# Optimization experiments

Hardware: AMD Instinct MI355X
Metric: run time of the kernel (lower is better)

Reference implementation:

```python
import jax, jax.numpy as jnp
import numpy as np

D_MODEL = 256; N_HEADS = 8; D_FFN = 1024; N_LEVELS = 4; N_POINTS = 4
HEAD_DIM = D_MODEL // N_HEADS
SHAPES = ((100, 100), (50, 50), (25, 25), (13, 13))  # static (H, W) per level
LEN_V = sum(h * w for h, w in SHAPES)  # 13294
BS = 8; NQ = 900


def layer_norm(x, g, b, eps=1e-5):
    m = x.mean(-1, keepdims=True)
    v = ((x - m) ** 2).mean(-1, keepdims=True)
    return (x - m) * jax.lax.rsqrt(v + eps) * g + b


def bilinear_sample(val, loc, H, W):
    # val: [bs, nH, H*W, hd]; loc: [bs, nq, nH, P, 2] normalized to [0,1].
    # Matches torch grid_sample(bilinear, zeros padding, align_corners=False)
    # with grid = 2*loc - 1, i.e. pixel coords x = loc_x*W - 0.5.
    bs, nq, nH, P, _ = loc.shape
    x = loc[..., 0] * W - 0.5
    y = loc[..., 1] * H - 0.5
    x0 = jnp.floor(x); y0 = jnp.floor(y)
    fx = x - x0; fy = y - y0  # grads flow to loc through fx/fy
    x0 = x0.astype(jnp.int32); y0 = y0.astype(jnp.int32)
    out = jnp.zeros((bs, nq, nH, P, HEAD_DIM), val.dtype)
    for dy, wy in ((0, 1.0 - fy), (1, fy)):
        for dx, wx in ((0, 1.0 - fx), (1, fx)):
            xi = x0 + dx; yi = y0 + dy
            valid = (xi >= 0) & (xi < W) & (yi >= 0) & (yi < H)
            idx = jnp.clip(yi, 0, H - 1) * W + jnp.clip(xi, 0, W - 1)  # [bs,nq,nH,P]
            idx = idx.transpose(0, 2, 1, 3).reshape(bs, nH, nq * P)
            g = jnp.take_along_axis(val, idx[..., None], axis=2)  # [bs,nH,nq*P,hd]
            g = g.reshape(bs, nH, nq, P, HEAD_DIM).transpose(0, 2, 1, 3, 4)
            w = (wx * wy * valid).astype(val.dtype)[..., None]
            out = out + g * w
    return out  # [bs, nq, nH, P, hd]


def setup_inputs() -> dict:
    key = jax.random.key(0)
    ks = jax.random.split(key, 16)
    d = D_MODEL
    w = lambda k, shape: (jax.random.normal(k, shape) * 0.02).astype(jnp.float32)
    z = lambda n: jnp.zeros((n,), jnp.float32)
    o = lambda n: jnp.ones((n,), jnp.float32)
    return {
        "embed": jax.random.normal(ks[0], (BS, NQ, d), jnp.float32),
        "refer_bbox": jax.random.uniform(ks[1], (BS, NQ, 4), jnp.float32),  # cxcywh in [0,1]
        "feats": jax.random.normal(ks[2], (BS, LEN_V, d), jnp.float32),
        "query_pos": jax.random.normal(ks[3], (BS, NQ, d), jnp.float32),
        "Wq": w(ks[4], (d, d)), "bq": z(d), "Wk": w(ks[5], (d, d)), "bk": z(d),
        "Wv": w(ks[6], (d, d)), "bv": z(d), "Wo": w(ks[7], (d, d)), "bo": z(d),
        "g1": o(d), "b1": z(d),
        "Wval": w(ks[8], (d, d)), "bval": z(d),
        "Woff": w(ks[9], (d, N_HEADS * N_LEVELS * N_POINTS * 2)), "boff": z(N_HEADS * N_LEVELS * N_POINTS * 2),
        "Waw": w(ks[10], (d, N_HEADS * N_LEVELS * N_POINTS)), "baw": z(N_HEADS * N_LEVELS * N_POINTS),
        "Wop": w(ks[11], (d, d)), "bop": z(d),
        "g2": o(d), "b2": z(d),
        "W1": w(ks[12], (d, D_FFN)), "bf1": z(D_FFN),
        "W2": w(ks[13], (D_FFN, d)), "bf2": z(d),
        "g3": o(d), "b3": z(d),
    }


def reference(embed, refer_bbox, feats, query_pos, Wq, bq, Wk, bk, Wv, bv, Wo, bo,
              g1, b1, Wval, bval, Woff, boff, Waw, baw, Wop, bop, g2, b2,
              W1, bf1, W2, bf2, g3, b3):
    bs, nq, d = embed.shape
    # ---- self attention (q = k = embed + query_pos, v = embed) ----
    qk_in = embed + query_pos
    q = (qk_in @ Wq + bq).reshape(bs, nq, N_HEADS, HEAD_DIM)
    k = (qk_in @ Wk + bk).reshape(bs, nq, N_HEADS, HEAD_DIM)
    v = (embed @ Wv + bv).reshape(bs, nq, N_HEADS, HEAD_DIM)
    scores = jnp.einsum('bqhd,bkhd->bhqk', q, k) * (HEAD_DIM ** -0.5)
    attn = jax.nn.softmax(scores, -1)
    sa = jnp.einsum('bhqk,bkhd->bqhd', attn, v).reshape(bs, nq, d) @ Wo + bo
    embed = layer_norm(embed + sa, g1, b1)
    # ---- MSDeformAttn cross attention ----
    query = embed + query_pos
    rb = refer_bbox[:, :, None, :]  # [bs, nq, 1, 4] (refer_bbox.unsqueeze(2))
    value = (feats @ Wval + bval).reshape(bs, LEN_V, N_HEADS, HEAD_DIM)
    off = (query @ Woff + boff).reshape(bs, nq, N_HEADS, N_LEVELS, N_POINTS, 2)
    aw = jax.nn.softmax((query @ Waw + baw).reshape(bs, nq, N_HEADS, N_LEVELS * N_POINTS), -1)
    aw = aw.reshape(bs, nq, N_HEADS, N_LEVELS, N_POINTS)
    # num_points == 4 branch: loc = cxcy + off/P * wh * 0.5
    loc = rb[:, :, None, :, None, :2] + off / N_POINTS * rb[:, :, None, :, None, 2:] * 0.5
    out = jnp.zeros((bs, nq, N_HEADS, HEAD_DIM), embed.dtype)
    start = 0
    for l, (H, W) in enumerate(SHAPES):
        val_l = value[:, start:start + H * W].transpose(0, 2, 1, 3)  # [bs,nH,HW,hd]
        s = bilinear_sample(val_l, loc[:, :, :, l], H, W)  # [bs,nq,nH,P,hd]
        out = out + (s * aw[:, :, :, l, :, None]).sum(3)
        start += H * W
    ca = out.reshape(bs, nq, d) @ Wop + bop
    embed = layer_norm(embed + ca, g2, b2)
    # ---- FFN ----
    ff = jax.nn.relu(embed @ W1 + bf1) @ W2 + bf2
    return layer_norm(embed + ff, g3, b3)
```

## Files before the change

kernel.cpp:

```cpp
#include <hip/hip_runtime.h>
#include <hip/hip_bf16.h>
#include <cstddef>

#define BS 8
#define NQ 900
#define DM 256
#define LEN_V 13294

using bf16x8 = __attribute__((ext_vector_type(8))) __bf16;
using f32x4  = __attribute__((ext_vector_type(4))) float;

__device__ __forceinline__ unsigned short f2bf(float f) {
    union { float f; unsigned int u; } v; v.f = f;
    unsigned int r = v.u + 0x7FFFu + ((v.u >> 16) & 1u);
    return (unsigned short)(r >> 16);
}
__device__ __forceinline__ float bf2f(unsigned short u) {
    union { unsigned int u; float f; } v; v.u = ((unsigned int)u) << 16;
    return v.f;
}

#define SW(r) (((r) + ((r) >> 2)) & 3)

#define FLAG_RELU 1
#define FLAG_OBF  2
#define FLAG_SWAP 4
#define FLAG_QKV  8

struct WDesc { const float* src; unsigned short* dst; int K; int N; float scale; };
struct WPrepArgs { WDesc w[10]; };

__global__ __launch_bounds__(256) void wprep_kernel(WPrepArgs args)
{
    WDesc d = args.w[blockIdx.z];
    int k0 = blockIdx.x * 32;
    int n0 = blockIdx.y * 32;
    if (k0 >= d.K || n0 >= d.N) return;
    __shared__ unsigned short t[32][33];
    int tx = threadIdx.x & 31, ty = threadIdx.x >> 5;
    #pragma unroll
    for (int i = 0; i < 4; ++i) {
        int kk = ty + i * 8;
        t[kk][tx] = f2bf(d.src[(size_t)(k0 + kk) * d.N + n0 + tx] * d.scale);
    }
    __syncthreads();
    #pragma unroll
    for (int i = 0; i < 4; ++i) {
        int nn = ty + i * 8;
        d.dst[(size_t)(n0 + nn) * d.K + k0 + tx] = t[tx][nn];
    }
}

__global__ __launch_bounds__(256) void bias_concat_kernel(
    const float* __restrict__ bq, const float* __restrict__ bk,
    const float* __restrict__ bv, const float* __restrict__ boff,
    const float* __restrict__ baw, float* __restrict__ bqkv,
    float* __restrict__ boffaw)
{
    const float sc = 0.17677669529663687f;
    int t = blockIdx.x * 256 + threadIdx.x;
    if (t < 256)       bqkv[t] = bq[t] * sc;
    else if (t < 512)  bqkv[t] = bk[t - 256];
    else if (t < 768)  bqkv[t] = bv[t - 512];
    if (t < 256)       boffaw[t] = boff[t];
    else if (t < 384)  boffaw[t] = baw[t - 256];
}

#define GLOADA(B, k0) do {                                                    \
    if constexpr (ABF) {                                                      \
        const unsigned short* ap_ = Abf + (size_t)agr * K + (k0) + ah;        \
        qa##B##0 = aok ? *(const uint4*)ap_ : z4;                             \
        qa##B##1 = aok ? *(const uint4*)(ap_ + 8) : z4;                       \
    } else {                                                                  \
        if (aok) {                                                            \
            const float* ap_ = Afp + (size_t)agr * K + (k0) + ah;             \
            pa##B##0 = *(const f32x4*)(ap_);                                  \
            pa##B##1 = *(const f32x4*)(ap_ + 4);                              \
            pa##B##2 = *(const f32x4*)(ap_ + 8);                              \
            pa##B##3 = *(const f32x4*)(ap_ + 12);                             \
            if (A2) {                                                         \
                const float* a2_ = A2 + (size_t)agr * K + (k0) + ah;          \
                pa##B##0 += *(const f32x4*)(a2_);                             \
                pa##B##1 += *(const f32x4*)(a2_ + 4);                         \
                pa##B##2 += *(const f32x4*)(a2_ + 8);                         \
                pa##B##3 += *(const f32x4*)(a2_ + 12);                        \
            }                                                                 \
        } else { pa##B##0 = zf4; pa##B##1 = zf4; pa##B##2 = zf4; pa##B##3 = zf4; } \
    }                                                                         \
    { const unsigned short* bp_ = BT + (size_t)bgr * K + (k0) + ah;           \
      pb##B##0 = *(const uint4*)bp_; pb##B##1 = *(const uint4*)(bp_ + 8); }   \
} while (0)

#define GSTAGE(B) do {                                                        \
    if constexpr (ABF) {                                                      \
        As4[ar * 4 + ((acb + 0) ^ SW(ar))] = qa##B##0;                        \
        As4[ar * 4 + ((acb + 1) ^ SW(ar))] = qa##B##1;                        \
    } else {                                                                  \
        union { unsigned short us_[8]; uint4 q_; } u0_, u1_;                  \
        u0_.us_[0] = f2bf(pa##B##0[0]); u0_.us_[1] = f2bf(pa##B##0[1]);       \
        u0_.us_[2] = f2bf(pa##B##0[2]); u0_.us_[3] = f2bf(pa##B##0[3]);       \
        u0_.us_[4] = f2bf(pa##B##1[0]); u0_.us_[5] = f2bf(pa##B##1[1]);       \
        u0_.us_[6] = f2bf(pa##B##1[2]); u0_.us_[7] = f2bf(pa##B##1[3]);       \
        u1_.us_[0] = f2bf(pa##B##2[0]); u1_.us_[1] = f2bf(pa##B##2[1]);       \
        u1_.us_[2] = f2bf(pa##B##2[2]); u1_.us_[3] = f2bf(pa##B##2[3]);       \
        u1_.us_[4] = f2bf(pa##B##3[0]); u1_.us_[5] = f2bf(pa##B##3[1]);       \
        u1_.us_[6] = f2bf(pa##B##3[2]); u1_.us_[7] = f2bf(pa##B##3[3]);       \
        As4[ar * 4 + ((acb + 0) ^ SW(ar))] = u0_.q_;                          \
        As4[ar * 4 + ((acb + 1) ^ SW(ar))] = u1_.q_;                          \
    }                                                                         \
    Bs4[ar * 4 + ((acb + 0) ^ SW(ar))] = pb##B##0;                            \
    Bs4[ar * 4 + ((acb + 1) ^ SW(ar))] = pb##B##1;                            \
} while (0)

#define GMFMA() do {                                                          \
    bf16x8 af[4], bfr[4];                                                     \
    _Pragma("unroll")                                                         \
    for (int mi = 0; mi < 4; ++mi) {                                          \
        int r = wm * 64 + mi * 16 + lr;                                       \
        af[mi] = Asb[r * 4 + (lc ^ SW(r))];                                   \
    }                                                                         \
    _Pragma("unroll")                                                         \
    for (int ni = 0; ni < 4; ++ni) {                                          \
        int r = wn * 64 + ni * 16 + lr;                                       \
        bfr[ni] = Bsb[r * 4 + (lc ^ SW(r))];                                  \
    }                                                                         \
    _Pragma("unroll")                                                         \
    for (int mi = 0; mi < 4; ++mi)                                            \
        _Pragma("unroll")                                                     \
        for (int ni = 0; ni < 4; ++ni)                                        \
            acc[mi][ni] = __builtin_amdgcn_mfma_f32_16x16x32_bf16(            \
                af[mi], bfr[ni], acc[mi][ni], 0, 0, 0);                       \
} while (0)

template<int ABF>
__global__ __launch_bounds__(256) void gemm_big(
    const void* __restrict__ Ain, const float* __restrict__ A2,
    const unsigned short* __restrict__ BT, const float* __restrict__ bias,
    void* __restrict__ Cout, int M, int N, int K, int flags)
{
    __shared__ uint4 SMEM[1088];
    uint4* As4 = SMEM;
    uint4* Bs4 = SMEM + 512;

    const int tid = threadIdx.x;
    const int lane = tid & 63;
    const int wave = tid >> 6;
    const int wm = wave >> 1;
    const int wn = wave & 1;
    const int row0 = (flags & FLAG_SWAP ? blockIdx.y : blockIdx.x) * 128;
    const int col0 = (flags & FLAG_SWAP ? blockIdx.x : blockIdx.y) * 128;
    if ((flags & FLAG_QKV) && col0 >= 512) A2 = nullptr;

    const float* Afp = (const float*)Ain;
    const unsigned short* Abf = (const unsigned short*)Ain;

    f32x4 acc[4][4];
    #pragma unroll
    for (int i = 0; i < 4; ++i)
        #pragma unroll
        for (int j = 0; j < 4; ++j)
            acc[i][j] = {0.f, 0.f, 0.f, 0.f};

    const int ar  = tid >> 1;
    const int ah  = (tid & 1) * 16;
    const int acb = (tid & 1) * 2;
    const int agr = row0 + ar;
    const bool aok = agr < M;
    const int bgr = col0 + ar;
    const int lr = lane & 15;
    const int lc = lane >> 4;

    const bf16x8* Asb = (const bf16x8*)As4;
    const bf16x8* Bsb = (const bf16x8*)Bs4;
    const uint4 z4 = {0u, 0u, 0u, 0u};
    const f32x4 zf4 = {0.f, 0.f, 0.f, 0.f};

    f32x4 pa00, pa01, pa02, pa03, pa10, pa11, pa12, pa13;
    uint4 qa00, qa01, qa10, qa11;
    uint4 pb00, pb01, pb10, pb11;

    const int nsteps = K >> 5;
    GLOADA(0, 0);
    for (int s = 0; s < nsteps; s += 2) {
        __syncthreads();
        GSTAGE(0);
        GLOADA(1, (s + 1 < nsteps ? (s + 1) * 32 : 0));
        __syncthreads();
        GMFMA();
        __syncthreads();
        GSTAGE(1);
        GLOADA(0, (s + 2 < nsteps ? (s + 2) * 32 : 0));
        __syncthreads();
        GMFMA();
    }

    const int relu = flags & FLAG_RELU;
    if (!(flags & FLAG_OBF)) {
        float* C = (float*)Cout;
        #pragma unroll
        for (int ni = 0; ni < 4; ++ni) {
            int col = col0 + wn * 64 + ni * 16 + lr;
            if (col >= N) continue;
            float bval = bias[col];
            #pragma unroll
            for (int mi = 0; mi < 4; ++mi) {
                #pragma unroll
                for (int rg = 0; rg < 4; ++rg) {
                    int row = row0 + wm * 64 + mi * 16 + lc * 4 + rg;
                    if (row < M) {
                        float o = acc[mi][ni][rg] + bval;
                        if (relu) o = fmaxf(o, 0.f);
                        C[(size_t)row * N + col] = o;
                    }
                }
            }
        }
    } else {
        unsigned short* RP = (unsigned short*)SMEM;
        unsigned short* C = (unsigned short*)Cout;
        float bval[4];
        #pragma unroll
        for (int ni = 0; ni < 4; ++ni) {
            int col = col0 + wn * 64 + ni * 16 + lr;
            bval[ni] = (col < N) ? bias[col] : 0.f;
        }
        #pragma unroll
        for (int h2 = 0; h2 < 2; ++h2) {
            __syncthreads();
            if (wm == h2) {
                #pragma unroll
                for (int ni = 0; ni < 4; ++ni) {
                    int colL = wn * 64 + ni * 16 + lr;
                    #pragma unroll
                    for (int mi = 0; mi < 4; ++mi) {
                        #pragma unroll
                        for (int rg = 0; rg < 4; ++rg) {
                            int rowL = mi * 16 + lc * 4 + rg;
                            float o = acc[mi][ni][rg] + bval[ni];
                            if (relu) o = fmaxf(o, 0.f);
                            RP[rowL * 136 + colL] = f2bf(o);
                        }
                    }
                }
            }
            __syncthreads();
            {
                int r = tid >> 2;
                int c = tid & 3;
                int grow = row0 + h2 * 64 + r;
                if (grow < M) {
                    #pragma unroll
                    for (int j = 0; j < 4; ++j) {
                        int gcol = col0 + c * 32 + j * 8;
                        if (gcol < N) {
                            uint4 vq = *(const uint4*)&RP[r * 136 + c * 32 + j * 8];
                            *(uint4*)(C + (size_t)grow * N + gcol) = vq;
                        }
                    }
                }
            }
        }
    }
}

#define SLOADA(B, k0) do {                                                    \
    if constexpr (ABF) {                                                      \
        const unsigned short* ap_ = Abf + (size_t)agr * K + (k0) + ah;        \
        qa##B = aok ? *(const uint4*)ap_ : z4;                                \
    } else {                                                                  \
        if (aok) {                                                            \
            const float* ap_ = Afp + (size_t)agr * K + (k0) + ah;             \
            pa##B##0 = *(const f32x4*)(ap_);                                  \
            pa##B##1 = *(const f32x4*)(ap_ + 4);                              \
            if (A2) {                                                         \
                const float* a2_ = A2 + (size_t)agr * K + (k0) + ah;          \
                pa##B##0 += *(const f32x4*)(a2_);                             \
                pa##B##1 += *(const f32x4*)(a2_ + 4);                         \
            }                                                                 \
        } else { pa##B##0 = zf4; pa##B##1 = zf4; }                            \
    }                                                                         \
    { const unsigned short* bp_ = BT + (size_t)bgr * K + (k0) + ah;           \
      pb##B = *(const uint4*)bp_; }                                           \
} while (0)

#define SSTAGE(B) do {                                                        \
    if constexpr (ABF) {                                                      \
        As4[ar * 4 + (ac ^ SW(ar))] = qa##B;                                  \
    } else {                                                                  \
        union { unsigned short us_[8]; uint4 q_; } u_;                        \
        u_.us_[0] = f2bf(pa##B##0[0]); u_.us_[1] = f2bf(pa##B##0[1]);         \
        u_.us_[2] = f2bf(pa##B##0[2]); u_.us_[3] = f2bf(pa##B##0[3]);         \
        u_.us_[4] = f2bf(pa##B##1[0]); u_.us_[5] = f2bf(pa##B##1[1]);         \
        u_.us_[6] = f2bf(pa##B##1[2]); u_.us_[7] = f2bf(pa##B##1[3]);         \
        As4[ar * 4 + (ac ^ SW(ar))] = u_.q_;                                  \
    }                                                                         \
    Bs4[ar * 4 + (ac ^ SW(ar))] = pb##B;                                      \
} while (0)

#define SMFMA() do {                                                          \
    bf16x8 af[2], bfr[2];                                                     \
    _Pragma("unroll")                                                         \
    for (int mi = 0; mi < 2; ++mi) {                                          \
        int r = wm * 32 + mi * 16 + lr;                                       \
        af[mi] = Asb[r * 4 + (lc ^ SW(r))];                                   \
    }                                                                         \
    _Pragma("unroll")                                                         \
    for (int ni = 0; ni < 2; ++ni) {                                          \
        int r = wn * 32 + ni * 16 + lr;                                       \
        bfr[ni] = Bsb[r * 4 + (lc ^ SW(r))];                                  \
    }                                                                         \
    _Pragma("unroll")                                                         \
    for (int mi = 0; mi < 2; ++mi)                                            \
        _Pragma("unroll")                                                     \
        for (int ni = 0; ni < 2; ++ni)                                        \
            acc[mi][ni] = __builtin_amdgcn_mfma_f32_16x16x32_bf16(            \
                af[mi], bfr[ni], acc[mi][ni], 0, 0, 0);                       \
} while (0)

template<int ABF>
__global__ __launch_bounds__(256) void gemm_small(
    const void* __restrict__ Ain, const float* __restrict__ A2,
    const unsigned short* __restrict__ BT, const float* __restrict__ bias,
    void* __restrict__ Cout, int M, int N, int K, int flags)
{
    __shared__ uint4 SMEM[512];
    uint4* As4 = SMEM;
    uint4* Bs4 = SMEM + 256;

    const int tid = threadIdx.x;
    const int lane = tid & 63;
    const int wave = tid >> 6;
    const int wm = wave >> 1;
    const int wn = wave & 1;
    const int row0 = (flags & FLAG_SWAP ? blockIdx.y : blockIdx.x) * 64;
    const int col0 = (flags & FLAG_SWAP ? blockIdx.x : blockIdx.y) * 64;
    if ((flags & FLAG_QKV) && col0 >= 512) A2 = nullptr;

    const float* Afp = (const float*)Ain;
    const unsigned short* Abf = (const unsigned short*)Ain;

    f32x4 acc[2][2];
    #pragma unroll
    for (int i = 0; i < 2; ++i)
        #pragma unroll
        for (int j = 0; j < 2; ++j)
            acc[i][j] = {0.f, 0.f, 0.f, 0.f};

    const int ar = tid >> 2;
    const int ac = tid & 3;
    const int ah = ac * 8;
    const int agr = row0 + ar;
    const bool aok = agr < M;
    const int bgr = col0 + ar;
    const int lr = lane & 15;
    const int lc = lane >> 4;

    const bf16x8* Asb = (const bf16x8*)As4;
    const bf16x8* Bsb = (const bf16x8*)Bs4;
    const uint4 z4 = {0u, 0u, 0u, 0u};
    const f32x4 zf4 = {0.f, 0.f, 0.f, 0.f};

    f32x4 pa00, pa01, pa10, pa11;
    uint4 qa0, qa1;
    uint4 pb0, pb1;

    const int nsteps = K >> 5;
    SLOADA(0, 0);
    for (int s = 0; s < nsteps; s += 2) {
        __syncthreads();
        SSTAGE(0);
        SLOADA(1, (s + 1 < nsteps ? (s + 1) * 32 : 0));
        __syncthreads();
        SMFMA();
        __syncthreads();
        SSTAGE(1);
        SLOADA(0, (s + 2 < nsteps ? (s + 2) * 32 : 0));
        __syncthreads();
        SMFMA();
    }

    const int relu = flags & FLAG_RELU;
    if (!(flags & FLAG_OBF)) {
        float* C = (float*)Cout;
        #pragma unroll
        for (int ni = 0; ni < 2; ++ni) {
            int col = col0 + wn * 32 + ni * 16 + lr;
            if (col >= N) continue;
            float bval = bias[col];
            #pragma unroll
            for (int mi = 0; mi < 2; ++mi) {
                #pragma unroll
                for (int rg = 0; rg < 4; ++rg) {
                    int row = row0 + wm * 32 + mi * 16 + lc * 4 + rg;
                    if (row < M) {
                        float o = acc[mi][ni][rg] + bval;
                        if (relu) o = fmaxf(o, 0.f);
                        C[(size_t)row * N + col] = o;
                    }
                }
            }
        }
    } else {
        unsigned short* RP = (unsigned short*)SMEM;
        unsigned short* C = (unsigned short*)Cout;
        float bval[2];
        #pragma unroll
        for (int ni = 0; ni < 2; ++ni) {
            int col = col0 + wn * 32 + ni * 16 + lr;
            bval[ni] = (col < N) ? bias[col] : 0.f;
        }
        #pragma unroll
        for (int h2 = 0; h2 < 2; ++h2) {
            __syncthreads();
            if (wm == h2) {
                #pragma unroll
                for (int ni = 0; ni < 2; ++ni) {
                    int colL = wn * 32 + ni * 16 + lr;
                    #pragma unroll
                    for (int mi = 0; mi < 2; ++mi) {
                        #pragma unroll
                        for (int rg = 0; rg < 4; ++rg) {
                            int rowL = mi * 16 + lc * 4 + rg;
                            float o = acc[mi][ni][rg] + bval[ni];
                            if (relu) o = fmaxf(o, 0.f);
                            RP[rowL * 72 + colL] = f2bf(o);
                        }
                    }
                }
            }
            __syncthreads();
            {
                int r = tid >> 3;
                int c = tid & 7;
                int grow = row0 + h2 * 32 + r;
                int gcol = col0 + c * 8;
                if (grow < M && gcol < N) {
                    uint4 vq = *(const uint4*)&RP[r * 72 + c * 8];
                    *(uint4*)(C + (size_t)grow * N + gcol) = vq;
                }
            }
        }
    }
}

#define QKVS 768
__global__ __launch_bounds__(256) void attn_mfma_kernel(
    const unsigned short* __restrict__ qkv, float* __restrict__ out)
{
    __shared__ uint4 Kls[64 * 4];
    __shared__ uint4 Vtls[32 * 8];

    const int tid = threadIdx.x;
    const int lane = tid & 63;
    const int wave = tid >> 6;
    const int qcol = lane & 15;
    const int g = lane >> 4;
    const int bh = blockIdx.x;
    const int h = bh & 7, b = bh >> 3;
    const int qg = blockIdx.y * 64 + wave * 16 + qcol;
    const int qc = qg < NQ ? qg : NQ - 1;

    bf16x8 qf = *(const bf16x8*)(qkv + ((size_t)(b * NQ + qc)) * QKVS + h * 32 + g * 8);

    float mrun = -3.0e38f, lrun = 0.f;
    f32x4 oacc[2];
    oacc[0] = {0.f, 0.f, 0.f, 0.f};
    oacc[1] = {0.f, 0.f, 0.f, 0.f};
    const f32x4 zacc = {0.f, 0.f, 0.f, 0.f};

    const int kidx = tid >> 2, kdc = tid & 3;
    const int vkp = tid >> 3, vdc = tid & 7;
    const bf16x8* Kb = (const bf16x8*)Kls;
    const bf16x8* Vb = (const bf16x8*)Vtls;
    unsigned int* V32 = (unsigned int*)Vtls;

    for (int jb = 0; jb < NQ; jb += 64) {
        __syncthreads();
        {
            int gk = jb + kidx;
            const uint4 z = {0u, 0u, 0u, 0u};
            uint4 kv = (gk < NQ)
                ? *(const uint4*)(qkv + ((size_t)(b * NQ + gk)) * QKVS + 256 + h * 32 + kdc * 8)
                : z;
            Kls[kidx * 4 + (kdc ^ ((kidx >> 1) & 3))] = kv;
        }
        {
            int k0g = jb + 2 * vkp;
            ushort4 a = {0, 0, 0, 0}, c = {0, 0, 0, 0};
            if (k0g < NQ)
                a = *(const ushort4*)(qkv + ((size_t)(b * NQ + k0g)) * QKVS + 512 + h * 32 + vdc * 4);
            if (k0g + 1 < NQ)
                c = *(const ushort4*)(qkv + ((size_t)(b * NQ + k0g + 1)) * QKVS + 512 + h * 32 + vdc * 4);
            unsigned int p0 = (unsigned int)a.x | ((unsigned int)c.x << 16);
            unsigned int p1 = (unsigned int)a.y | ((unsigned int)c.y << 16);
            unsigned int p2 = (unsigned int)a.z | ((unsigned int)c.z << 16);
            unsigned int p3 = (unsigned int)a.w | ((unsigned int)c.w << 16);
            int d0 = vdc * 4;
            V32[(d0+0) * 32 + ((vkp >> 2) ^ ((d0+0) & 7)) * 4 + (vkp & 3)] = p0;
            V32[(d0+1) * 32 + ((vkp >> 2) ^ ((d0+1) & 7)) * 4 + (vkp & 3)] = p1;
            V32[(d0+2) * 32 + ((vkp >> 2) ^ ((d0+2) & 7)) * 4 + (vkp & 3)] = p2;
            V32[(d0+3) * 32 + ((vkp >> 2) ^ ((d0+3) & 7)) * 4 + (vkp & 3)] = p3;
        }
        __syncthreads();

        f32x4 sacc[4];
        #pragma unroll
        for (int kt = 0; kt < 4; ++kt) {
            int key = kt * 16 + qcol;
            bf16x8 kf = Kb[key * 4 + (g ^ ((key >> 1) & 3))];
            sacc[kt] = __builtin_amdgcn_mfma_f32_16x16x32_bf16(kf, qf, zacc, 0, 0, 0);
        }
        if (jb + 64 > NQ) {
            #pragma unroll
            for (int kt = 0; kt < 4; ++kt)
                #pragma unroll
                for (int r = 0; r < 4; ++r)
                    if (jb + kt * 16 + 4 * g + r >= NQ) sacc[kt][r] = -3.0e38f;
        }

        float mloc = -3.0e38f;
        #pragma unroll
        for (int kt = 0; kt < 4; ++kt)
            #pragma unroll
            for (int r = 0; r < 4; ++r)
                mloc = fmaxf(mloc, sacc[kt][r]);
        mloc = fmaxf(mloc, __shfl_xor(mloc, 16));
        mloc = fmaxf(mloc, __shfl_xor(mloc, 32));
        float mnew = fmaxf(mrun, mloc);
        float corr = __expf(mrun - mnew);
        mrun = mnew;

        float lloc = 0.f;
        unsigned int pk2[4][2];
        #pragma unroll
        for (int kt = 0; kt < 4; ++kt) {
            float p0 = __expf(sacc[kt][0] - mnew);
            float p1 = __expf(sacc[kt][1] - mnew);
            float p2 = __expf(sacc[kt][2] - mnew);
            float p3 = __expf(sacc[kt][3] - mnew);
            lloc += p0 + p1 + p2 + p3;
            pk2[kt][0] = (unsigned int)f2bf(p0) | ((unsigned int)f2bf(p1) << 16);
            pk2[kt][1] = (unsigned int)f2bf(p2) | ((unsigned int)f2bf(p3) << 16);
        }
        lloc += __shfl_xor(lloc, 16);
        lloc += __shfl_xor(lloc, 32);
        lrun = lrun * corr + lloc;
        #pragma unroll
        for (int ni = 0; ni < 2; ++ni)
            #pragma unroll
            for (int r = 0; r < 4; ++r)
                oacc[ni][r] *= corr;

        const int s0 = qcol + 32 * (g & 1);
        const bool hi = (g >> 1) != 0;
        #pragma unroll
        for (int tp = 0; tp < 2; ++tp) {
            int A0 = (int)pk2[2 * tp][0], A1 = (int)pk2[2 * tp][1];
            int B0 = (int)pk2[2 * tp + 1][0], B1 = (int)pk2[2 * tp + 1][1];
            int a0 = __shfl(A0, s0),      a1 = __shfl(A1, s0);
            int b0 = __shfl(B0, s0),      b1 = __shfl(B1, s0);
            int a2 = __shfl(A0, s0 + 16), a3 = __shfl(A1, s0 + 16);
            int b2 = __shfl(B0, s0 + 16), b3 = __shfl(B1, s0 + 16);
            union { unsigned int u[4]; bf16x8 v8; } pf;
            pf.u[0] = hi ? (unsigned int)b0 : (unsigned int)a0;
            pf.u[1] = hi ? (unsigned int)b1 : (unsigned int)a1;
            pf.u[2] = hi ? (unsigned int)b2 : (unsigned int)a2;
            pf.u[3] = hi ? (unsigned int)b3 : (unsigned int)a3;
            #pragma unroll
            for (int ni = 0; ni < 2; ++ni) {
                int d = ni * 16 + qcol;
                bf16x8 vf = Vb[d * 8 + ((4 * tp + g) ^ (d & 7))];
                oacc[ni] = __builtin_amdgcn_mfma_f32_16x16x32_bf16(vf, pf.v8, oacc[ni], 0, 0, 0);
            }
        }
    }

    if (qg < NQ) {
        float inv = 1.f / lrun;
        float* op = out + ((size_t)(b * NQ + qg)) * DM + h * 32;
        float4 o0, o1;
        o0.x = oacc[0][0] * inv; o0.y = oacc[0][1] * inv;
        o0.z = oacc[0][2] * inv; o0.w = oacc[0][3] * inv;
        o1.x = oacc[1][0] * inv; o1.y = oacc[1][1] * inv;
        o1.z = oacc[1][2] * inv; o1.w = oacc[1][3] * inv;
        *(float4*)(op + 4 * g) = o0;
        *(float4*)(op + 16 + 4 * g) = o1;
    }
}

__global__ __launch_bounds__(256) void aw_softmax_kernel(float* __restrict__ offaw)
{
    int t = blockIdx.x * 256 + threadIdx.x;
    if (t >= BS * NQ * 8) return;
    int row = t >> 3, h = t & 7;
    float* p = offaw + (size_t)row * 384 + 256 + h * 16;
    float vals[16];
    #pragma unroll
    for (int i = 0; i < 4; ++i) {
        float4 f = *(const float4*)(p + i * 4);
        vals[4 * i + 0] = f.x; vals[4 * i + 1] = f.y;
        vals[4 * i + 2] = f.z; vals[4 * i + 3] = f.w;
    }
    float mx = vals[0];
    #pragma unroll
    for (int i = 1; i < 16; ++i) mx = fmaxf(mx, vals[i]);
    float sum = 0.f;
    #pragma unroll
    for (int i = 0; i < 16; ++i) { vals[i] = __expf(vals[i] - mx); sum += vals[i]; }
    float inv = 1.f / sum;
    #pragma unroll
    for (int i = 0; i < 4; ++i) {
        float4 f;
        f.x = vals[4 * i + 0] * inv; f.y = vals[4 * i + 1] * inv;
        f.z = vals[4 * i + 2] * inv; f.w = vals[4 * i + 3] * inv;
        *(float4*)(p + i * 4) = f;
    }
}

__global__ __launch_bounds__(256) void deform_kernel(
    const unsigned short* __restrict__ value, const float* __restrict__ offaw,
    const float* __restrict__ rbbox, float* __restrict__ dout)
{
    int t = blockIdx.x * 256 + threadIdx.x;
    if (t >= BS * NQ * 64) return;
    int c = t & 7;
    int h = (t >> 3) & 7;
    int bq = t >> 6;
    int b = bq / NQ;

    const int Hs[4]     = {100, 50, 25, 13};
    const int Wsz[4]    = {100, 50, 25, 13};
    const int Starts[4] = {0, 10000, 12500, 13125};

    float4 rb = *(const float4*)(rbbox + (size_t)bq * 4);
    const float* offp = offaw + (size_t)bq * 384 + h * 32;
    const float* awp  = offaw + (size_t)bq * 384 + 256 + h * 16;
    const unsigned short* vb = value + ((size_t)b * LEN_V) * 256 + h * 32 + c * 4;

    float4 acc = make_float4(0.f, 0.f, 0.f, 0.f);
    #pragma unroll
    for (int l = 0; l < 4; ++l) {
        const int H = Hs[l], W = Wsz[l], st = Starts[l];
        #pragma unroll
        for (int p = 0; p < 4; ++p) {
            float ox = offp[l * 8 + p * 2 + 0];
            float oy = offp[l * 8 + p * 2 + 1];
            float a_w = awp[l * 4 + p];
            float xx = (rb.x + ox * 0.125f * rb.z) * W - 0.5f;
            float yy = (rb.y + oy * 0.125f * rb.w) * H - 0.5f;
            float x0f = floorf(xx), y0f = floorf(yy);
            float fx = xx - x0f, fy = yy - y0f;
            int x0 = (int)x0f, y0 = (int)y0f;
            #pragma unroll
            for (int dy = 0; dy < 2; ++dy) {
                int yi = y0 + dy;
                float wy = dy ? fy : (1.f - fy);
                bool vy = (yi >= 0) && (yi < H);
                int yc = min(max(yi, 0), H - 1);
                #pragma unroll
                for (int dx = 0; dx < 2; ++dx) {
                    int xi = x0 + dx;
                    float wx = dx ? fx : (1.f - fx);
                    bool vx = (xi >= 0) && (xi < W);
                    int xc = min(max(xi, 0), W - 1);
                    float wgt = a_w * wy * wx * ((vx && vy) ? 1.f : 0.f);
                    ushort4 gv = *(const ushort4*)(vb + (size_t)(st + yc * W + xc) * 256);
                    acc.x += wgt * bf2f(gv.x); acc.y += wgt * bf2f(gv.y);
                    acc.z += wgt * bf2f(gv.z); acc.w += wgt * bf2f(gv.w);
                }
            }
        }
    }
    *(float4*)(dout + (size_t)bq * 256 + h * 32 + c * 4) = acc;
}

__global__ __launch_bounds__(256) void ln_kernel(
    const float* __restrict__ x, const float* __restrict__ dx,
    const float* __restrict__ g, const float* __restrict__ bt,
    float* __restrict__ out, int rows)
{
    int row = blockIdx.x * 4 + (threadIdx.x >> 6);
    if (row >= rows) return;
    int lane = threadIdx.x & 63;
    size_t base = (size_t)row * 256 + lane * 4;
    float4 xv = *(const float4*)(x + base);
    float4 dv = *(const float4*)(dx + base);
    float a0 = xv.x + dv.x, a1 = xv.y + dv.y, a2 = xv.z + dv.z, a3 = xv.w + dv.w;
    float s = a0 + a1 + a2 + a3;
    float s2 = a0 * a0 + a1 * a1 + a2 * a2 + a3 * a3;
    #pragma unroll
    for (int o = 32; o; o >>= 1) {
        s += __shfl_xor(s, o);
        s2 += __shfl_xor(s2, o);
    }
    float mean = s * (1.f / 256.f);
    float var = s2 * (1.f / 256.f) - mean * mean;
    float inv = rsqrtf(var + 1e-5f);
    float4 gv = *(const float4*)(g + lane * 4);
    float4 bv = *(const float4*)(bt + lane * 4);
    float4 r;
    r.x = (a0 - mean) * inv * gv.x + bv.x;
    r.y = (a1 - mean) * inv * gv.y + bv.y;
    r.z = (a2 - mean) * inv * gv.z + bv.z;
    r.w = (a3 - mean) * inv * gv.w + bv.w;
    *(float4*)(out + base) = r;
}

extern "C" void kernel_launch(void* const* d_in, const int* in_sizes, int n_in,
                              void* d_out, int out_size, void* d_ws, size_t ws_size,
                              hipStream_t stream)
{
    const float* embed = (const float*)d_in[0];
    const float* rbbox = (const float*)d_in[1];
    const float* feats = (const float*)d_in[2];
    const float* qpos  = (const float*)d_in[3];
    const float* Wq = (const float*)d_in[4];  const float* bq = (const float*)d_in[5];
    const float* Wk = (const float*)d_in[6];  const float* bk = (const float*)d_in[7];
    const float* Wv = (const float*)d_in[8];  const float* bv = (const float*)d_in[9];
    const float* Wo = (const float*)d_in[10]; const float* bo = (const float*)d_in[11];
    const float* g1 = (const float*)d_in[12]; const float* b1 = (const float*)d_in[13];
    const float* Wval = (const float*)d_in[14]; const float* bval = (const float*)d_in[15];
    const float* Woff = (const float*)d_in[16]; const float* boff = (const float*)d_in[17];
    const float* Waw  = (const float*)d_in[18]; const float* baw  = (const float*)d_in[19];
    const float* Wop  = (const float*)d_in[20]; const float* bop  = (const float*)d_in[21];
    const float* g2 = (const float*)d_in[22]; const float* b2 = (const float*)d_in[23];
    const float* W1 = (const float*)d_in[24]; const float* bf1 = (const float*)d_in[25];
    const float* W2 = (const float*)d_in[26]; const float* bf2 = (const float*)d_in[27];
    const float* g3 = (const float*)d_in[28]; const float* b3 = (const float*)d_in[29];

    const int M = BS * NQ;
    const int MV = BS * LEN_V;
    const size_t E = (size_t)M * DM;
    const size_t VAL = (size_t)MV * DM;

    float* ws = (float*)d_ws;
    float* valueb = ws;
    float* qkvreg = ws + VAL;
    float* attb   = qkvreg + 3 * E;
    float* e1b    = attb + E;
    unsigned short* wbase = (unsigned short*)(e1b + E);
    unsigned short* wqkv_t   = wbase;
    unsigned short* wo_t     = wbase + 196608;
    unsigned short* wval_t   = wbase + 262144;
    unsigned short* woffaw_t = wbase + 327680;
    unsigned short* wop_t    = wbase + 425984;
    unsigned short* w1_t     = wbase + 491520;
    unsigned short* w2_t     = wbase + 753664;
    float* bqkv   = (float*)(wbase + 1015808);
    float* boffaw = bqkv + 768;

    unsigned short* valuebf = (unsigned short*)valueb;
    unsigned short* qkvbf   = (unsigned short*)qkvreg;
    float* sab    = qkvreg;
    float* offawb = qkvreg + E;
    float* doutb  = attb;
    float* cab    = qkvreg;
    float* e2b    = qkvreg + 2 * E;
    unsigned short* ffhb = (unsigned short*)valueb;
    float* ffb    = attb;

    dim3 blk(256);
    auto gsB = [](int m, int n) { return dim3((n + 127) / 128, (m + 127) / 128); };
    auto gsS = [](int m, int n) { return dim3((n + 63) / 64, (m + 63) / 64); };

    {
        const float sc = 0.17677669529663687f;
        WPrepArgs a;
        a.w[0] = {Wq,   wqkv_t,                 256, 256,  sc};
        a.w[1] = {Wk,   wqkv_t + 256 * 256,     256, 256,  1.f};
        a.w[2] = {Wv,   wqkv_t + 512 * 256,     256, 256,  1.f};
        a.w[3] = {Wo,   wo_t,                   256, 256,  1.f};
        a.w[4] = {Wval, wval_t,                 256, 256,  1.f};
        a.w[5] = {Woff, woffaw_t,               256, 256,  1.f};
        a.w[6] = {Waw,  woffaw_t + 256 * 256,   256, 128,  1.f};
        a.w[7] = {Wop,  wop_t,                  256, 256,  1.f};
        a.w[8] = {W1,   w1_t,                   256, 1024, 1.f};
        a.w[9] = {W2,   w2_t,                   1024, 256, 1.f};
        wprep_kernel<<<dim3(32, 32, 10), blk, 0, stream>>>(a);
        bias_concat_kernel<<<dim3(3), blk, 0, stream>>>(bq, bk, bv, boff, baw, bqkv, boffaw);
    }

    gemm_small<0><<<gsS(M, 768), blk, 0, stream>>>(embed, qpos, wqkv_t, bqkv, qkvbf, M, 768, 256, FLAG_SWAP | FLAG_QKV | FLAG_OBF);
    attn_mfma_kernel<<<dim3(BS * 8, (NQ + 63) / 64), blk, 0, stream>>>(qkvbf, attb);
    gemm_small<0><<<gsS(M, 256), blk, 0, stream>>>(attb, nullptr, wo_t, bo, sab, M, 256, 256, FLAG_SWAP);
    ln_kernel<<<dim3((M + 3) / 4), blk, 0, stream>>>(embed, sab, g1, b1, e1b, M);
    gemm_big<0><<<gsB(MV, 256), blk, 0, stream>>>(feats, nullptr, wval_t, bval, valuebf, MV, 256, 256, FLAG_SWAP | FLAG_OBF);
    gemm_small<0><<<gsS(M, 384), blk, 0, stream>>>(e1b, qpos, woffaw_t, boffaw, offawb, M, 384, 256, FLAG_SWAP);
    aw_softmax_kernel<<<dim3((BS * NQ * 8 + 255) / 256), blk, 0, stream>>>(offawb);
    deform_kernel<<<dim3((BS * NQ * 64 + 255) / 256), blk, 0, stream>>>(valuebf, offawb, rbbox, doutb);
    gemm_small<0><<<gsS(M, 256), blk, 0, stream>>>(doutb, nullptr, wop_t, bop, cab, M, 256, 256, FLAG_SWAP);
    ln_kernel<<<dim3((M + 3) / 4), blk, 0, stream>>>(e1b, cab, g2, b2, e2b, M);
    gemm_small<0><<<gsS(M, 1024), blk, 0, stream>>>(e2b, nullptr, w1_t, bf1, ffhb, M, 1024, 256, FLAG_SWAP | FLAG_RELU | FLAG_OBF);
    gemm_small<1><<<gsS(M, 256), blk, 0, stream>>>(ffhb, nullptr, w2_t, bf2, ffb, M, 256, 1024, FLAG_SWAP);
    ln_kernel<<<dim3((M + 3) / 4), blk, 0, stream>>>(e2b, ffb, g3, b3, (float*)d_out, M);
}
```

Baseline: 250.9 us.

## Stage value-projection GEMM operands via direct global-to-LDS DMA with double buffering

Replaces the generic gemm_big used for the value projection with a specialised gemm_val. It loads fp32 A tiles and bf16 B tiles straight into LDS using global_load_lds, double-buffered across two LDS stages with XOR swizzling. The fp32-to-bf16 conversion moves from the staging step to the MFMA fragment read. The goal is to cut register staging and VGPR pressure and to overlap the next tile's loads with the current MFMAs. In exchange, LDS use grows (48KB), every step now fully drains vmcnt, and A is stored as fp32 in LDS, which doubles the LDS read traffic for A.

```diff
diff --git a/kernel.cpp b/kernel.cpp
--- a/kernel.cpp
+++ b/kernel.cpp
@@ -26,6 +26,15 @@
 #define FLAG_OBF  2
 #define FLAG_SWAP 4
 #define FLAG_QKV  8
+
+#define AS1(p) ((const __attribute__((address_space(1))) void*)(p))
+#define AS3(p) ((__attribute__((address_space(3))) void*)(p))
+
+#define DRAIN_DMA() do {                                   \
+    __builtin_amdgcn_sched_barrier(0);                     \
+    asm volatile("s_waitcnt vmcnt(0)" ::: "memory");       \
+    __builtin_amdgcn_sched_barrier(0);                     \
+} while (0)
 
 struct WDesc { const float* src; unsigned short* dst; int K; int N; float scale; };
 struct WPrepArgs { WDesc w[10]; };
@@ -66,93 +75,20 @@
     else if (t < 384)  boffaw[t] = baw[t - 256];
 }
 
-#define GLOADA(B, k0) do {                                                    \
-    if constexpr (ABF) {                                                      \
-        const unsigned short* ap_ = Abf + (size_t)agr * K + (k0) + ah;        \
-        qa##B##0 = aok ? *(const uint4*)ap_ : z4;                             \
-        qa##B##1 = aok ? *(const uint4*)(ap_ + 8) : z4;                       \
-    } else {                                                                  \
-        if (aok) {                                                            \
-            const float* ap_ = Afp + (size_t)agr * K + (k0) + ah;             \
-            pa##B##0 = *(const f32x4*)(ap_);                                  \
-            pa##B##1 = *(const f32x4*)(ap_ + 4);                              \
-            pa##B##2 = *(const f32x4*)(ap_ + 8);                              \
-            pa##B##3 = *(const f32x4*)(ap_ + 12);                             \
-            if (A2) {                                                         \
-                const float* a2_ = A2 + (size_t)agr * K + (k0) + ah;          \
-                pa##B##0 += *(const f32x4*)(a2_);                             \
-                pa##B##1 += *(const f32x4*)(a2_ + 4);                         \
-                pa##B##2 += *(const f32x4*)(a2_ + 8);                         \
-                pa##B##3 += *(const f32x4*)(a2_ + 12);                        \
-            }                                                                 \
-        } else { pa##B##0 = zf4; pa##B##1 = zf4; pa##B##2 = zf4; pa##B##3 = zf4; } \
-    }                                                                         \
-    { const unsigned short* bp_ = BT + (size_t)bgr * K + (k0) + ah;           \
-      pb##B##0 = *(const uint4*)bp_; pb##B##1 = *(const uint4*)(bp_ + 8); }   \
-} while (0)
-
-#define GSTAGE(B) do {                                                        \
-    if constexpr (ABF) {                                                      \
-        As4[ar * 4 + ((acb + 0) ^ SW(ar))] = qa##B##0;                        \
-        As4[ar * 4 + ((acb + 1) ^ SW(ar))] = qa##B##1;                        \
-    } else {                                                                  \
-        union { unsigned short us_[8]; uint4 q_; } u0_, u1_;                  \
-        u0_.us_[0] = f2bf(pa##B##0[0]); u0_.us_[1] = f2bf(pa##B##0[1]);       \
-        u0_.us_[2] = f2bf(pa##B##0[2]); u0_.us_[3] = f2bf(pa##B##0[3]);       \
-        u0_.us_[4] = f2bf(pa##B##1[0]); u0_.us_[5] = f2bf(pa##B##1[1]);       \
-        u0_.us_[6] = f2bf(pa##B##1[2]); u0_.us_[7] = f2bf(pa##B##1[3]);       \
-        u1_.us_[0] = f2bf(pa##B##2[0]); u1_.us_[1] = f2bf(pa##B##2[1]);       \
-        u1_.us_[2] = f2bf(pa##B##2[2]); u1_.us_[3] = f2bf(pa##B##2[3]);       \
-        u1_.us_[4] = f2bf(pa##B##3[0]); u1_.us_[5] = f2bf(pa##B##3[1]);       \
-        u1_.us_[6] = f2bf(pa##B##3[2]); u1_.us_[7] = f2bf(pa##B##3[3]);       \
-        As4[ar * 4 + ((acb + 0) ^ SW(ar))] = u0_.q_;                          \
-        As4[ar * 4 + ((acb + 1) ^ SW(ar))] = u1_.q_;                          \
-    }                                                                         \
-    Bs4[ar * 4 + ((acb + 0) ^ SW(ar))] = pb##B##0;                            \
-    Bs4[ar * 4 + ((acb + 1) ^ SW(ar))] = pb##B##1;                            \
-} while (0)
-
-#define GMFMA() do {                                                          \
-    bf16x8 af[4], bfr[4];                                                     \
-    _Pragma("unroll")                                                         \
-    for (int mi = 0; mi < 4; ++mi) {                                          \
-        int r = wm * 64 + mi * 16 + lr;                                       \
-        af[mi] = Asb[r * 4 + (lc ^ SW(r))];                                   \
-    }                                                                         \
-    _Pragma("unroll")                                                         \
-    for (int ni = 0; ni < 4; ++ni) {                                          \
-        int r = wn * 64 + ni * 16 + lr;                                       \
-        bfr[ni] = Bsb[r * 4 + (lc ^ SW(r))];                                  \
-    }                                                                         \
-    _Pragma("unroll")                                                         \
-    for (int mi = 0; mi < 4; ++mi)                                            \
-        _Pragma("unroll")                                                     \
-        for (int ni = 0; ni < 4; ++ni)                                        \
-            acc[mi][ni] = __builtin_amdgcn_mfma_f32_16x16x32_bf16(            \
-                af[mi], bfr[ni], acc[mi][ni], 0, 0, 0);                       \
-} while (0)
-
-template<int ABF>
-__global__ __launch_bounds__(256) void gemm_big(
-    const void* __restrict__ Ain, const float* __restrict__ A2,
-    const unsigned short* __restrict__ BT, const float* __restrict__ bias,
-    void* __restrict__ Cout, int M, int N, int K, int flags)
-{
-    __shared__ uint4 SMEM[1088];
-    uint4* As4 = SMEM;
-    uint4* Bs4 = SMEM + 512;
+__global__ __launch_bounds__(256) void gemm_val(
+    const float* __restrict__ A, const unsigned short* __restrict__ BT,
+    const float* __restrict__ bias, unsigned short* __restrict__ C,
+    int M, int N, int K)
+{
+    __shared__ uint4 SMEM[3072];
 
     const int tid = threadIdx.x;
     const int lane = tid & 63;
     const int wave = tid >> 6;
     const int wm = wave >> 1;
     const int wn = wave & 1;
-    const int row0 = (flags & FLAG_SWAP ? blockIdx.y : blockIdx.x) * 128;
-    const int col0 = (flags & FLAG_SWAP ? blockIdx.x : blockIdx.y) * 128;
-    if ((flags & FLAG_QKV) && col0 >= 512) A2 = nullptr;
-
-    const float* Afp = (const float*)Ain;
-    const unsigned short* Abf = (const unsigned short*)Ain;
+    const int row0 = blockIdx.y * 128;
+    const int col0 = blockIdx.x * 128;
 
     f32x4 acc[4][4];
     #pragma unroll
@@ -161,63 +97,78 @@
         for (int j = 0; j < 4; ++j)
             acc[i][j] = {0.f, 0.f, 0.f, 0.f};
 
-    const int ar  = tid >> 1;
-    const int ah  = (tid & 1) * 16;
-    const int acb = (tid & 1) * 2;
-    const int agr = row0 + ar;
-    const bool aok = agr < M;
-    const int bgr = col0 + ar;
     const int lr = lane & 15;
     const int lc = lane >> 4;
 
-    const bf16x8* Asb = (const bf16x8*)As4;
-    const bf16x8* Bsb = (const bf16x8*)Bs4;
-    const uint4 z4 = {0u, 0u, 0u, 0u};
-    const f32x4 zf4 = {0.f, 0.f, 0.f, 0.f};
-
-    f32x4 pa00, pa01, pa02, pa03, pa10, pa11, pa12, pa13;
-    uint4 qa00, qa01, qa10, qa11;
-    uint4 pb00, pb01, pb10, pb11;
-
-    const int nsteps = K >> 5;
-    GLOADA(0, 0);
-    for (int s = 0; s < nsteps; s += 2) {
+    const int achunk = (lane & 7) ^ ((lane >> 3) & 7);
+    const int bchunk = (lane & 3) ^ ((lane >> 2) & 3);
+
+    auto STAGE = [&](int k0, int buf) {
+        uint4* Ab = SMEM + buf * 1536;
+        uint4* Bb = Ab + 1024;
+        #pragma unroll
+        for (int c = 0; c < 4; ++c) {
+            int r = wave * 32 + c * 8 + (lane >> 3);
+            int gr = row0 + r; if (gr >= M) gr = M - 1;
+            const float* g = A + (size_t)gr * K + k0 + achunk * 4;
+            __builtin_amdgcn_global_load_lds(AS1(g), AS3(Ab + (wave * 4 + c) * 64), 16, 0, 0);
+        }
+        #pragma unroll
+        for (int c = 0; c < 2; ++c) {
+            int r = wave * 32 + c * 16 + (lane >> 2);
+            const unsigned short* g = BT + (size_t)(col0 + r) * K + k0 + bchunk * 8;
+            __builtin_amdgcn_global_load_lds(AS1(g), AS3(Bb + (wave * 2 + c) * 64), 16, 0, 0);
+        }
+    };
+
+    auto MSTEP = [&](int buf) {
+        const float* Af = (const float*)(SMEM + buf * 1536);
+        const bf16x8* Bb8 = (const bf16x8*)(SMEM + buf * 1536 + 1024);
+        bf16x8 af[4], bfr[4];
+        #pragma unroll
+        for (int mi = 0; mi < 4; ++mi) {
+            int R = wm * 64 + mi * 16 + lr;
+            int s0 = (2 * lc) ^ (R & 7);
+            int s1 = (2 * lc + 1) ^ (R & 7);
+            f32x4 a0 = *(const f32x4*)(Af + R * 32 + s0 * 4);
+            f32x4 a1 = *(const f32x4*)(Af + R * 32 + s1 * 4);
+            union { unsigned short us[8]; bf16x8 v; } u;
+            u.us[0] = f2bf(a0[0]); u.us[1] = f2bf(a0[1]);
+            u.us[2] = f2bf(a0[2]); u.us[3] = f2bf(a0[3]);
+            u.us[4] = f2bf(a1[0]); u.us[5] = f2bf(a1[1]);
+            u.us[6] = f2bf(a1[2]); u.us[7] = f2bf(a1[3]);
+            af[mi] = u.v;
+        }
+        #pragma unroll
+        for (int ni = 0; ni < 4; ++ni) {
+            int R = wn * 64 + ni * 16 + lr;
+            bfr[ni] = Bb8[R * 4 + (lc ^ (R & 3))];
+        }
+        #pragma unroll
+        for (int mi = 0; mi < 4; ++mi)
+            #pragma unroll
+            for (int ni = 0; ni < 4; ++ni)
+                acc[mi][ni] = __builtin_amdgcn_mfma_f32_16x16x32_bf16(
+                    af[mi], bfr[ni], acc[mi][ni], 0, 0, 0);
+    };
+
+    const int NS = K >> 5;
+    STAGE(0, 0);
+    DRAIN_DMA();
+    __syncthreads();
+    for (int s = 0; s < NS; s += 2) {
+        if (s + 1 < NS) STAGE((s + 1) * 32, 1);
+        MSTEP(0);
+        DRAIN_DMA();
         __syncthreads();
-        GSTAGE(0);
-        GLOADA(1, (s + 1 < nsteps ? (s + 1) * 32 : 0));
+        if (s + 2 < NS) STAGE((s + 2) * 32, 0);
+        MSTEP(1);
+        DRAIN_DMA();
         __syncthreads();
-        GMFMA();
-        __syncthreads();
-        GSTAGE(1);
-        GLOADA(0, (s + 2 < nsteps ? (s + 2) * 32 : 0));
-        __syncthreads();
-        GMFMA();
-    }
-
-    const int relu = flags & FLAG_RELU;
-    if (!(flags & FLAG_OBF)) {
-        float* C = (float*)Cout;
-        #pragma unroll
-        for (int ni = 0; ni < 4; ++ni) {
-            int col = col0 + wn * 64 + ni * 16 + lr;
-            if (col >= N) continue;
-            float bval = bias[col];
-            #pragma unroll
-            for (int mi = 0; mi < 4; ++mi) {
-                #pragma unroll
-                for (int rg = 0; rg < 4; ++rg) {
-                    int row = row0 + wm * 64 + mi * 16 + lc * 4 + rg;
-                    if (row < M) {
-                        float o = acc[mi][ni][rg] + bval;
-                        if (relu) o = fmaxf(o, 0.f);
-                        C[(size_t)row * N + col] = o;
-                    }
-                }
-            }
-        }
-    } else {
+    }
+
+    {
         unsigned short* RP = (unsigned short*)SMEM;
-        unsigned short* C = (unsigned short*)Cout;
         float bval[4];
         #pragma unroll
         for (int ni = 0; ni < 4; ++ni) {
@@ -236,9 +187,7 @@
                         #pragma unroll
                         for (int rg = 0; rg < 4; ++rg) {
                             int rowL = mi * 16 + lc * 4 + rg;
-                            float o = acc[mi][ni][rg] + bval[ni];
-                            if (relu) o = fmaxf(o, 0.f);
-                            RP[rowL * 136 + colL] = f2bf(o);
+                            RP[rowL * 136 + colL] = f2bf(acc[mi][ni][rg] + bval[ni]);
                         }
                     }
                 }
@@ -252,10 +201,8 @@
                     #pragma unroll
                     for (int j = 0; j < 4; ++j) {
                         int gcol = col0 + c * 32 + j * 8;
-                        if (gcol < N) {
-                            uint4 vq = *(const uint4*)&RP[r * 136 + c * 32 + j * 8];
-                            *(uint4*)(C + (size_t)grow * N + gcol) = vq;
-                        }
+                        uint4 vq = *(const uint4*)&RP[r * 136 + c * 32 + j * 8];
+                        *(uint4*)(C + (size_t)grow * N + gcol) = vq;
                     }
                 }
             }
@@ -760,7 +707,6 @@
     float* ffb    = attb;
 
     dim3 blk(256);
-    auto gsB = [](int m, int n) { return dim3((n + 127) / 128, (m + 127) / 128); };
     auto gsS = [](int m, int n) { return dim3((n + 63) / 64, (m + 63) / 64); };
 
     {
@@ -784,7 +730,7 @@
     attn_mfma_kernel<<<dim3(BS * 8, (NQ + 63) / 64), blk, 0, stream>>>(qkvbf, attb);
     gemm_small<0><<<gsS(M, 256), blk, 0, stream>>>(attb, nullptr, wo_t, bo, sab, M, 256, 256, FLAG_SWAP);
     ln_kernel<<<dim3((M + 3) / 4), blk, 0, stream>>>(embed, sab, g1, b1, e1b, M);
-    gemm_big<0><<<gsB(MV, 256), blk, 0, stream>>>(feats, nullptr, wval_t, bval, valuebf, MV, 256, 256, FLAG_SWAP | FLAG_OBF);
+    gemm_val<<<dim3(2, (MV + 127) / 128), blk, 0, stream>>>(feats, wval_t, bval, valuebf, MV, 256, 256);
     gemm_small<0><<<gsS(M, 384), blk, 0, stream>>>(e1b, qpos, woffaw_t, boffaw, offawb, M, 384, 256, FLAG_SWAP);
     aw_softmax_kernel<<<dim3((BS * NQ * 8 + 255) / 256), blk, 0, stream>>>(offawb);
     deform_kernel<<<dim3((BS * NQ * 64 + 255) / 256), blk, 0, stream>>>(valuebf, offawb, rbbox, doutb);
```

After: 245.6 us. 2.1% less time.
